# Performance work log

Measured on AMD Instinct MI355X. Metric: run time of the kernel, lower is better.

## Reference

```python
import jax, jax.numpy as jnp
import numpy as np

B = 128          # graphs
NPG = 512        # nodes per graph
N = B * NPG      # total nodes
DEG = 8
E = N * DEG      # total edges (intra-graph)
D = 100          # num_feature_dim / num_node_labels
HID = 128        # config.hidden
HEADS = 8
F1 = 20          # per-head dim of first GATConv in each GATNet
RATIO = 0.5
K = int(np.ceil(RATIO * NPG))  # nodes kept per graph by SAGPooling
NEG_SLOPE = 0.2


def setup_inputs() -> dict:
    key = jax.random.key(0)
    ks = jax.random.split(key, 24)
    x = jax.random.randint(ks[0], (N,), 0, D)
    # intra-graph random edges: local ids in [0, NPG) + graph offset
    src_l = jax.random.randint(ks[1], (B, NPG * DEG), 0, NPG)
    dst_l = jax.random.randint(ks[2], (B, NPG * DEG), 0, NPG)
    off = (jnp.arange(B) * NPG)[:, None]
    edge_index = jnp.stack([(src_l + off).ravel(), (dst_l + off).ravel()])
    batch = jnp.repeat(jnp.arange(B), NPG)

    def lin(k, fan_in, fan_out):
        return jax.random.normal(k, (fan_in, fan_out), jnp.float32) / np.sqrt(fan_in)

    def att(k, h, f):
        return jax.random.normal(k, (h, f), jnp.float32) * 0.1

    p = {
        # GATNet A (conv1): GATConv(D, 20, heads=8) then GATConv(160, HID, heads=1)
        "W_a1": lin(ks[3], D, HEADS * F1), "asrc_a1": att(ks[4], HEADS, F1),
        "adst_a1": att(ks[5], HEADS, F1), "b_a1": jnp.zeros((HEADS * F1,), jnp.float32),
        "W_a2": lin(ks[6], HEADS * F1, HID), "asrc_a2": att(ks[7], 1, HID),
        "adst_a2": att(ks[8], 1, HID), "b_a2": jnp.zeros((HID,), jnp.float32),
        # GATNet B (conv4): GATConv(HID, 20, heads=8) then GATConv(160, HID, heads=1)
        "W_b1": lin(ks[9], HID, HEADS * F1), "asrc_b1": att(ks[10], HEADS, F1),
        "adst_b1": att(ks[11], HEADS, F1), "b_b1": jnp.zeros((HEADS * F1,), jnp.float32),
        "W_b2": lin(ks[12], HEADS * F1, HID), "asrc_b2": att(ks[13], 1, HID),
        "adst_b2": att(ks[14], 1, HID), "b_b2": jnp.zeros((HID,), jnp.float32),
        # SAGPooling GraphConv(HID, 1)
        "w_rel": lin(ks[15], HID, 1), "w_root": lin(ks[16], HID, 1),
        "b_pool": jnp.zeros((1,), jnp.float32),
    }
    return {"x": x, "edge_index": edge_index, "batch": batch, **p}


def _gat_conv(h, src, dst, W, asrc, adst, b):
    """PyG GATConv (with self-loops already included in src/dst)."""
    Hh, Ff = asrc.shape
    z = (h @ W).reshape(N, Hh, Ff)                       # [N,H,F]
    es = jnp.sum(z * asrc, axis=-1)                      # [N,H] source logits
    ed = jnp.sum(z * adst, axis=-1)                      # [N,H] dest logits
    e = jax.nn.leaky_relu(es[src] + ed[dst], NEG_SLOPE)  # [E',H]
    m = jax.ops.segment_max(e, dst, num_segments=N)
    m = jnp.where(jnp.isfinite(m), m, 0.0)
    ex = jnp.exp(e - m[dst])
    den = jax.ops.segment_sum(ex, dst, num_segments=N)
    alpha = ex / (den[dst] + 1e-16)
    out = jax.ops.segment_sum(z[src] * alpha[:, :, None], dst, num_segments=N)
    return out.reshape(N, Hh * Ff) + b


def reference(x, edge_index, batch,
              W_a1, asrc_a1, adst_a1, b_a1, W_a2, asrc_a2, adst_a2, b_a2,
              W_b1, asrc_b1, adst_b1, b_b1, W_b2, asrc_b2, adst_b2, b_b2,
              w_rel, w_root, b_pool):
    src, dst = edge_index[0], edge_index[1]
    loops = jnp.arange(N)
    src_sl = jnp.concatenate([src, loops])  # GATConv adds self loops
    dst_sl = jnp.concatenate([dst, loops])

    h = jax.nn.one_hot(x, D, dtype=jnp.float32)
    # GATNet A: conv1 -> relu -> conv2 ; outer relu (dropout is eval no-op)
    h = jax.nn.relu(_gat_conv(h, src_sl, dst_sl, W_a1, asrc_a1, adst_a1, b_a1))
    h = _gat_conv(h, src_sl, dst_sl, W_a2, asrc_a2, adst_a2, b_a2)
    h = jax.nn.relu(h)
    # GATNet B
    h = jax.nn.relu(_gat_conv(h, src_sl, dst_sl, W_b1, asrc_b1, adst_b1, b_b1))
    h = _gat_conv(h, src_sl, dst_sl, W_b2, asrc_b2, adst_b2, b_b2)
    h = jax.nn.relu(h)

    # SAGPooling: GraphConv(HID,1) score (no self loops), tanh, per-graph top-k
    nbr = jax.ops.segment_sum(h[src], dst, num_segments=N)
    score = jnp.tanh(nbr @ w_rel + h @ w_root + b_pool).ravel()   # [N]
    sv, si = jax.lax.top_k(score.reshape(B, NPG), K)              # [B,K]
    perm = (si + (jnp.arange(B) * NPG)[:, None]).ravel()          # global node ids
    x_sel = h[perm] * sv.ravel()[:, None]                         # [B*K, HID]
    pooled = jnp.max(x_sel.reshape(B, K, HID), axis=1)            # global_max_pool
    batch_out = jnp.repeat(jnp.arange(B), K)
    return (pooled, perm, sv.ravel(), batch_out)
```

## Files before the change

kernel.cpp:

```cpp
#include <hip/hip_runtime.h>
#include <math.h>

#define N_NODES 65536
#define NPG     512
#define NGRAPH  128
#define E_EDGES 524288
#define MAXDEG  64
#define NHEADS  8
#define F1      20
#define HID     128
#define D160    160
#define KSEL    256
#define NLBL    100

typedef unsigned short ushort_t;
typedef unsigned int   uint_t;
typedef unsigned long long u64;
typedef __attribute__((ext_vector_type(8))) short short8;
typedef __attribute__((ext_vector_type(4))) float f32x4;

__device__ __forceinline__ float lrelu(float x){ return x > 0.f ? x : 0.2f*x; }
__device__ __forceinline__ ushort_t f2bf(float f){
    uint_t u = __float_as_uint(f);
    return (ushort_t)((u + 0x7FFFu + ((u >> 16) & 1u)) >> 16);
}
__device__ __forceinline__ float bf2f(ushort_t u){ return __uint_as_float(((uint_t)u) << 16); }
__device__ __forceinline__ float bflo(uint_t v){ return __uint_as_float(v << 16); }
__device__ __forceinline__ float bfhi(uint_t v){ return __uint_as_float(v & 0xFFFF0000u); }
__device__ __forceinline__ int xswz(int bid, int nblocks){
    return (bid & 7) * (nblocks >> 3) + (bid >> 3);
}
__device__ __forceinline__ float rdlanef(float v, int i){
    return __uint_as_float((uint_t)__builtin_amdgcn_readlane(__float_as_int(v), i));
}

__device__ __forceinline__ u64 comp_make(float s, int idx){
    uint_t u = __float_as_uint(s);
    u ^= (u & 0x80000000u) ? 0xFFFFFFFFu : 0x80000000u;
    return ((u64)u << 32) | (u64)(511 - idx);
}
__device__ __forceinline__ float comp_score(u64 c){
    uint_t u = (uint_t)(c >> 32);
    u ^= (u & 0x80000000u) ? 0x80000000u : 0xFFFFFFFFu;
    return __uint_as_float(u);
}
__device__ __forceinline__ int comp_idx(u64 c){ return 511 - (int)(c & 0x1FFu); }
__device__ __forceinline__ u64 shfl_xor_u64(u64 x, int m){
    uint_t lo = __shfl_xor((uint_t)x, m);
    uint_t hi = __shfl_xor((uint_t)(x >> 32), m);
    return ((u64)hi << 32) | lo;
}

__global__ void k_zero(uint4* __restrict__ p){
    p[blockIdx.x*blockDim.x + threadIdx.x] = (uint4){0,0,0,0};
}

__global__ void k_build_ell(const int* __restrict__ src, const int* __restrict__ dst,
                            int* __restrict__ deg, int* __restrict__ ell){
    int blk = xswz(blockIdx.x, E_EDGES/256);
    int e = blk*blockDim.x + threadIdx.x;
    int d = dst[e];
    int p = atomicAdd(&deg[d], 1);
    if(p < MAXDEG) ell[d*MAXDEG + p] = src[e];
}

__global__ void k_prep_a(const float* __restrict__ W, const float* __restrict__ asrc,
                         const float* __restrict__ adst,
                         ushort_t* __restrict__ Wbf, float* __restrict__ esT,
                         float* __restrict__ edT){
    int lbl = blockIdx.x;
    int f = threadIdx.x;
    const float* wrow = W + lbl*D160;
    Wbf[lbl*D160 + f] = f2bf(wrow[f]);
    if(f < 16){
        int h = f & 7;
        const float* av = ((f < 8) ? asrc : adst) + h*F1;
        float s = 0.f;
        #pragma unroll
        for(int k=0; k<F1; ++k) s += wrow[h*F1 + k]*av[k];
        if(f < 8) esT[lbl*8 + h] = s;
        else      edT[lbl*8 + h] = s;
    }
}

__global__ __launch_bounds__(256) void k_attn8_a(const int* __restrict__ x,
        const int* __restrict__ deg, const int* __restrict__ ell,
        const ushort_t* __restrict__ Wbf, const float* __restrict__ esT,
        const float* __restrict__ edT, const float* __restrict__ bias,
        ushort_t* __restrict__ out){
    __shared__ __align__(16) ushort_t Wl[NLBL*D160];
    __shared__ float esL[NLBL*8], edL[NLBL*8];
    int tid = threadIdx.x;
    for(int i = tid; i < NLBL*D160/8; i += 256)
        ((uint4*)Wl)[i] = ((const uint4*)Wbf)[i];
    for(int i = tid; i < NLBL*8; i += 256){ esL[i] = esT[i]; edL[i] = edT[i]; }
    __syncthreads();
    int blk = xswz(blockIdx.x, N_NODES*NHEADS/256);
    int t = blk*256 + tid;
    int n = t >> 3, h = t & 7;
    int dg = deg[n]; if(dg > MAXDEG) dg = MAXDEG;
    int lbl = x[n];
    float edn = edL[lbl*8 + h];
    float wself = expf(lrelu(esL[lbl*8 + h] + edn));
    float den = wself;
    float acc[F1];
    {
        const uint_t* zn = (const uint_t*)Wl + lbl*80 + h*10;
        #pragma unroll
        for(int f=0; f<10; ++f){
            uint_t v = zn[f];
            acc[2*f]   = wself*bflo(v);
            acc[2*f+1] = wself*bfhi(v);
        }
    }
    const int* el = ell + n*MAXDEG;
    int i = 0;
    for(; i+2 <= dg; i += 2){
        int sa = el[i], sb = el[i+1];
        int la = x[sa], lb = x[sb];
        float wa = expf(lrelu(esL[la*8 + h] + edn));
        float wb = expf(lrelu(esL[lb*8 + h] + edn));
        den += wa + wb;
        const uint_t* za = (const uint_t*)Wl + la*80 + h*10;
        const uint_t* zb = (const uint_t*)Wl + lb*80 + h*10;
        #pragma unroll
        for(int f=0; f<10; ++f){
            uint_t va = za[f], vb = zb[f];
            acc[2*f]   += wa*bflo(va) + wb*bflo(vb);
            acc[2*f+1] += wa*bfhi(va) + wb*bfhi(vb);
        }
    }
    if(i < dg){
        int sa = el[i];
        int la = x[sa];
        float wa = expf(lrelu(esL[la*8 + h] + edn));
        den += wa;
        const uint_t* za = (const uint_t*)Wl + la*80 + h*10;
        #pragma unroll
        for(int f=0; f<10; ++f){
            uint_t va = za[f];
            acc[2*f]   += wa*bflo(va);
            acc[2*f+1] += wa*bfhi(va);
        }
    }
    float inv = 1.f/(den + 1e-16f);
    uint_t* o = (uint_t*)(out + (size_t)n*D160 + h*F1);
    const float* bb = bias + h*F1;
    #pragma unroll
    for(int f=0; f<10; ++f){
        float v0 = fmaxf(acc[2*f]*inv   + bb[2*f],   0.f);
        float v1 = fmaxf(acc[2*f+1]*inv + bb[2*f+1], 0.f);
        o[f] = (uint_t)f2bf(v0) | ((uint_t)f2bf(v1) << 16);
    }
}

__global__ void k_attn8(const int* __restrict__ deg, const int* __restrict__ ell,
                        const ushort_t* __restrict__ z8, const float* __restrict__ es8,
                        const float* __restrict__ ed8, const float* __restrict__ bias,
                        ushort_t* __restrict__ out){
    int blk = xswz(blockIdx.x, N_NODES*NHEADS/256);
    int t = blk*blockDim.x + threadIdx.x;
    int n = t >> 3, h = t & 7;
    int dg = deg[n]; if(dg > MAXDEG) dg = MAXDEG;
    float edn = ed8[t];
    float wself = expf(lrelu(es8[t] + edn));
    float den = wself;
    float acc[F1];
    const uint_t* zn = (const uint_t*)(z8 + (size_t)n*D160 + h*F1);
    #pragma unroll
    for(int f=0; f<10; ++f){
        uint_t v = zn[f];
        acc[2*f]   = wself*bflo(v);
        acc[2*f+1] = wself*bfhi(v);
    }
    const int* el = ell + n*MAXDEG;
    int i = 0;
    for(; i+2 <= dg; i += 2){
        int sa = el[i], sb = el[i+1];
        float ea = es8[sa*NHEADS + h], eb = es8[sb*NHEADS + h];
        const uint_t* za = (const uint_t*)(z8 + (size_t)sa*D160 + h*F1);
        const uint_t* zb = (const uint_t*)(z8 + (size_t)sb*D160 + h*F1);
        float wa = expf(lrelu(ea + edn));
        float wb = expf(lrelu(eb + edn));
        den += wa + wb;
        #pragma unroll
        for(int f=0; f<10; ++f){
            uint_t va = za[f], vb = zb[f];
            acc[2*f]   += wa*bflo(va) + wb*bflo(vb);
            acc[2*f+1] += wa*bfhi(va) + wb*bfhi(vb);
        }
    }
    if(i < dg){
        int sa = el[i];
        float ea = es8[sa*NHEADS + h];
        const uint_t* za = (const uint_t*)(z8 + (size_t)sa*D160 + h*F1);
        float wa = expf(lrelu(ea + edn));
        den += wa;
        #pragma unroll
        for(int f=0; f<10; ++f){
            uint_t va = za[f];
            acc[2*f]   += wa*bflo(va);
            acc[2*f+1] += wa*bfhi(va);
        }
    }
    float inv = 1.f/(den + 1e-16f);
    uint_t* o = (uint_t*)(out + (size_t)n*D160 + h*F1);
    const float* bb = bias + h*F1;
    #pragma unroll
    for(int f=0; f<10; ++f){
        float v0 = fmaxf(acc[2*f]*inv   + bb[2*f],   0.f);
        float v1 = fmaxf(acc[2*f+1]*inv + bb[2*f+1], 0.f);
        o[f] = (uint_t)f2bf(v0) | ((uint_t)f2bf(v1) << 16);
    }
}

template<int IN, int OUT, bool DOT>
__global__ __launch_bounds__(256) void k_gemm_mfma(const ushort_t* __restrict__ A,
                                                   const float* __restrict__ W,
                                                   ushort_t* __restrict__ C,
                                                   const float* __restrict__ va,
                                                   const float* __restrict__ vb,
                                                   float* __restrict__ oa,
                                                   float* __restrict__ ob){
    constexpr int NT = OUT/16;
    constexpr int KS = IN/32;
    constexpr int LDW = IN + 8;
    __shared__ __align__(16) ushort_t Wt[OUT*LDW];
    int tid = threadIdx.x;
    for(int i = tid; i < IN*OUT; i += 256){
        int k = i / OUT, n = i - k*OUT;
        Wt[n*LDW + k] = f2bf(W[i]);
    }
    __syncthreads();
    int blk = xswz(blockIdx.x, N_NODES/64);
    int wave = tid >> 6, lane = tid & 63;
    int col16 = lane & 15;
    int kq = (lane >> 4) * 8;
    int row = blk*64 + wave*16 + col16;
    const ushort_t* Ar = A + (size_t)row*IN + kq;
    f32x4 acc[NT];
    #pragma unroll
    for(int c=0;c<NT;++c) acc[c] = (f32x4){0.f,0.f,0.f,0.f};
    #pragma unroll
    for(int ks=0; ks<KS; ++ks){
        short8 af = *reinterpret_cast<const short8*>(Ar + ks*32);
        #pragma unroll
        for(int c=0;c<NT;++c){
            short8 bf = *reinterpret_cast<const short8*>(&Wt[(c*16 + col16)*LDW + ks*32 + kq]);
            acc[c] = __builtin_amdgcn_mfma_f32_16x16x32_bf16(af, bf, acc[c], 0, 0, 0);
        }
    }
    int rbase = blk*64 + wave*16 + (lane >> 4)*4;
    #pragma unroll
    for(int c=0;c<NT;++c){
        #pragma unroll
        for(int r=0;r<4;++r){
            C[(size_t)(rbase + r)*OUT + c*16 + col16] = f2bf(acc[c][r]);
        }
    }
    if(DOT){
        float pa[4] = {0,0,0,0}, pb[4] = {0,0,0,0};
        #pragma unroll
        for(int c=0;c<NT;++c){
            float a = va[c*16 + col16];
            float b = vb[c*16 + col16];
            #pragma unroll
            for(int r=0;r<4;++r){ pa[r] += acc[c][r]*a; pb[r] += acc[c][r]*b; }
        }
        #pragma unroll
        for(int o=1;o<16;o<<=1){
            #pragma unroll
            for(int r=0;r<4;++r){ pa[r] += __shfl_xor(pa[r], o); pb[r] += __shfl_xor(pb[r], o); }
        }
        if(col16 == 0){
            #pragma unroll
            for(int r=0;r<4;++r){ oa[rbase + r] = pa[r]; ob[rbase + r] = pb[r]; }
        }
    }
}

__global__ __launch_bounds__(256) void k_gemm_b1(const ushort_t* __restrict__ A,
                                                 const float* __restrict__ W,
                                                 const float* __restrict__ asrc,
                                                 const float* __restrict__ adst,
                                                 ushort_t* __restrict__ C,
                                                 float* __restrict__ es8,
                                                 float* __restrict__ ed8){
    constexpr int IN = HID, OUTW = D160, NT = 11, KS = IN/32, LDW = IN + 8;
    __shared__ __align__(16) ushort_t Wt[(OUTW+16)*LDW];
    int tid = threadIdx.x;
    for(int i = tid; i < IN*OUTW; i += 256){
        int k = i / OUTW, n = i - k*OUTW;
        Wt[n*LDW + k] = f2bf(W[i]);
    }
    for(int i = tid; i < IN*16; i += 256){
        int k = i >> 4, j = i & 15;
        const float* av = (j < 8 ? asrc : adst) + (j & 7)*F1;
        const float* wr = W + k*OUTW + (j & 7)*F1;
        float s = 0.f;
        #pragma unroll
        for(int f=0; f<F1; ++f) s += wr[f]*av[f];
        Wt[(OUTW + j)*LDW + k] = f2bf(s);
    }
    __syncthreads();
    int blk = xswz(blockIdx.x, N_NODES/64);
    int wave = tid >> 6, lane = tid & 63;
    int col16 = lane & 15;
    int kq = (lane >> 4) * 8;
    int row = blk*64 + wave*16 + col16;
    const ushort_t* Ar = A + (size_t)row*IN + kq;
    f32x4 acc[NT];
    #pragma unroll
    for(int c=0;c<NT;++c) acc[c] = (f32x4){0.f,0.f,0.f,0.f};
    #pragma unroll
    for(int ks=0; ks<KS; ++ks){
        short8 af = *reinterpret_cast<const short8*>(Ar + ks*32);
        #pragma unroll
        for(int c=0;c<NT;++c){
            short8 bf = *reinterpret_cast<const short8*>(&Wt[(c*16 + col16)*LDW + ks*32 + kq]);
            acc[c] = __builtin_amdgcn_mfma_f32_16x16x32_bf16(af, bf, acc[c], 0, 0, 0);
        }
    }
    int rbase = blk*64 + wave*16 + (lane >> 4)*4;
    #pragma unroll
    for(int c=0;c<10;++c){
        #pragma unroll
        for(int r=0;r<4;++r){
            C[(size_t)(rbase + r)*OUTW + c*16 + col16] = f2bf(acc[c][r]);
        }
    }
    #pragma unroll
    for(int r=0;r<4;++r){
        float v = acc[10][r];
        if(col16 < 8) es8[(size_t)(rbase + r)*8 + col16] = v;
        else          ed8[(size_t)(rbase + r)*8 + (col16 - 8)] = v;
    }
}

template<typename OutT, bool DOT>
__global__ void k_attn1(const int* __restrict__ deg, const int* __restrict__ ell,
                        const ushort_t* __restrict__ Z, const float* __restrict__ es,
                        const float* __restrict__ ed, const float* __restrict__ bias,
                        OutT* __restrict__ out,
                        const float* __restrict__ wa, const float* __restrict__ wb,
                        float* __restrict__ oa, float* __restrict__ ob){
    int blk = xswz(blockIdx.x, N_NODES/4);
    int gt = blk*blockDim.x + threadIdx.x;
    int n = gt >> 6;
    int l = threadIdx.x & 63;
    int dg = deg[n]; if(dg > MAXDEG) dg = MAXDEG;
    float edn = ed[n];
    float wself = expf(lrelu(es[n] + edn));
    int s_l = 0; float w_l = 0.f;
    if(l < dg){ s_l = ell[n*MAXDEG + l]; w_l = expf(lrelu(es[s_l] + edn)); }
    float den = w_l;
    for(int o=32;o>0;o>>=1) den += __shfl_xor(den,o);
    den += wself;
    const uint_t* Zu = (const uint_t*)Z;
    uint_t zn = Zu[(size_t)n*64 + l];
    float acc0 = wself*bflo(zn);
    float acc1 = wself*bfhi(zn);
    int i = 0;
    for(; i+4 <= dg; i += 4){
        int s0 = __builtin_amdgcn_readlane(s_l, i);
        int s1 = __builtin_amdgcn_readlane(s_l, i+1);
        int s2 = __builtin_amdgcn_readlane(s_l, i+2);
        int s3 = __builtin_amdgcn_readlane(s_l, i+3);
        uint_t z0 = Zu[(size_t)s0*64 + l];
        uint_t z1 = Zu[(size_t)s1*64 + l];
        uint_t z2 = Zu[(size_t)s2*64 + l];
        uint_t z3 = Zu[(size_t)s3*64 + l];
        float w0 = rdlanef(w_l, i);
        float w1 = rdlanef(w_l, i+1);
        float w2 = rdlanef(w_l, i+2);
        float w3 = rdlanef(w_l, i+3);
        acc0 += w0*bflo(z0) + w1*bflo(z1);
        acc1 += w0*bfhi(z0) + w1*bfhi(z1);
        acc0 += w2*bflo(z2) + w3*bflo(z3);
        acc1 += w2*bfhi(z2) + w3*bfhi(z3);
    }
    for(; i < dg; ++i){
        int s0 = __builtin_amdgcn_readlane(s_l, i);
        float w0 = rdlanef(w_l, i);
        uint_t z0 = Zu[(size_t)s0*64 + l];
        acc0 += w0*bflo(z0);
        acc1 += w0*bfhi(z0);
    }
    float inv = 1.f/(den + 1e-16f);
    float2 bb = ((const float2*)bias)[l];
    float r0 = fmaxf(acc0*inv + bb.x, 0.f);
    float r1 = fmaxf(acc1*inv + bb.y, 0.f);
    if(sizeof(OutT) == 2){
        ((uint_t*)out)[(size_t)n*64 + l] = (uint_t)f2bf(r0) | ((uint_t)f2bf(r1) << 16);
    } else {
        float2 rv; rv.x = r0; rv.y = r1;
        ((float2*)out)[(size_t)n*64 + l] = rv;
    }
    if(DOT){
        float2 a2 = ((const float2*)wa)[l];
        float2 b2 = ((const float2*)wb)[l];
        float pa = r0*a2.x + r1*a2.y;
        float pb = r0*b2.x + r1*b2.y;
        for(int o=32;o>0;o>>=1){ pa += __shfl_xor(pa,o); pb += __shfl_xor(pb,o); }
        if(l==0){ oa[n] = pa; ob[n] = pb; }
    }
}

__global__ void k_score(const int* __restrict__ deg, const int* __restrict__ ell,
                        const float* __restrict__ yrel, const float* __restrict__ rroot,
                        const float* __restrict__ bpool, float* __restrict__ score){
    int blk = xswz(blockIdx.x, N_NODES/256);
    int n = blk*blockDim.x + threadIdx.x;
    int dg = deg[n]; if(dg > MAXDEG) dg = MAXDEG;
    float s = rroot[n] + bpool[0];
    const int* el = ell + n*MAXDEG;
    int i = 0;
    for(; i+4 <= dg; i += 4){
        float y0 = yrel[el[i]],   y1 = yrel[el[i+1]];
        float y2 = yrel[el[i+2]], y3 = yrel[el[i+3]];
        s += (y0 + y1) + (y2 + y3);
    }
    for(; i < dg; ++i) s += yrel[el[i]];
    score[n] = tanhf(s);
}

__global__ __launch_bounds__(512) void k_topk_pool(const float* __restrict__ score,
                                                   const ushort_t* __restrict__ H,
                                                   float* __restrict__ pooled,
                                                   float* __restrict__ perm_f,
                                                   float* __restrict__ sv,
                                                   float* __restrict__ batch_f){
    __shared__ int   sidx[KSEL];
    __shared__ float sval[KSEL];
    __shared__ float pmax[512];
    int g = xswz(blockIdx.x, NGRAPH);
    int base = g*NPG;
    int t = threadIdx.x;
    if(t < 64){
        int l = t;
        u64 v[8];
        #pragma unroll
        for(int r=0;r<8;++r){
            int i = r*64 + l;
            v[r] = comp_make(score[base + i], i);
        }
        #pragma unroll
        for(int kk=1; kk<=9; ++kk){
            int k = 1 << kk;
            #pragma unroll
            for(int jj=kk-1; jj>=0; --jj){
                int j = 1 << jj;
                if(j < 64){
                    bool lower = (l & j) == 0;
                    #pragma unroll
                    for(int r=0;r<8;++r){
                        int i = r*64 + l;
                        u64 p = shfl_xor_u64(v[r], j);
                        bool desc = (i & k) == 0;
                        u64 mx = v[r] > p ? v[r] : p;
                        u64 mn = v[r] > p ? p : v[r];
                        v[r] = (lower == desc) ? mx : mn;
                    }
                } else {
                    int jr = j >> 6;
                    #pragma unroll
                    for(int r=0;r<8;++r){
                        if((r & jr) == 0){
                            int rp = r | jr;
                            int i = r*64 + l;
                            bool desc = (i & k) == 0;
                            u64 a = v[r], b = v[rp];
                            u64 mx = a > b ? a : b;
                            u64 mn = a > b ? b : a;
                            v[r]  = desc ? mx : mn;
                            v[rp] = desc ? mn : mx;
                        }
                    }
                }
            }
        }
        #pragma unroll
        for(int r=0;r<4;++r){
            int i = r*64 + l;
            int idx = comp_idx(v[r]);
            float s = comp_score(v[r]);
            perm_f[g*KSEL + i]  = (float)(base + idx);
            sv[g*KSEL + i]      = s;
            batch_f[g*KSEL + i] = (float)g;
            sidx[i] = idx; sval[i] = s;
        }
    }
    __syncthreads();
    int c = t & 127, kc = t >> 7;
    float mx = -1e30f;
    for(int kk = kc*64; kk < kc*64 + 64; ++kk){
        mx = fmaxf(mx, bf2f(H[(size_t)(base + sidx[kk])*HID + c]) * sval[kk]);
    }
    pmax[t] = mx;
    __syncthreads();
    if(t < HID){
        pooled[g*HID + t] = fmaxf(fmaxf(pmax[t], pmax[t+128]),
                                  fmaxf(pmax[t+256], pmax[t+384]));
    }
}

extern "C" void kernel_launch(void* const* d_in, const int* in_sizes, int n_in,
                              void* d_out, int out_size, void* d_ws, size_t ws_size,
                              hipStream_t stream) {
    const int*   x       = (const int*)  d_in[0];
    const int*   eidx    = (const int*)  d_in[1];
    const float* W_a1    = (const float*)d_in[3];
    const float* asrc_a1 = (const float*)d_in[4];
    const float* adst_a1 = (const float*)d_in[5];
    const float* b_a1    = (const float*)d_in[6];
    const float* W_a2    = (const float*)d_in[7];
    const float* asrc_a2 = (const float*)d_in[8];
    const float* adst_a2 = (const float*)d_in[9];
    const float* b_a2    = (const float*)d_in[10];
    const float* W_b1    = (const float*)d_in[11];
    const float* asrc_b1 = (const float*)d_in[12];
    const float* adst_b1 = (const float*)d_in[13];
    const float* b_b1    = (const float*)d_in[14];
    const float* W_b2    = (const float*)d_in[15];
    const float* asrc_b2 = (const float*)d_in[16];
    const float* adst_b2 = (const float*)d_in[17];
    const float* b_b2    = (const float*)d_in[18];
    const float* w_rel   = (const float*)d_in[19];
    const float* w_root  = (const float*)d_in[20];
    const float* b_pool  = (const float*)d_in[21];

    const int* e_src = eidx;
    const int* e_dst = eidx + E_EDGES;

    char* ws = (char*)d_ws;
    size_t off = 0;
    auto alloc = [&](size_t bytes)->char*{
        char* p = ws + off;
        off += (bytes + 255) & ~(size_t)255;
        return p;
    };
    int*      deg   = (int*)     alloc((size_t)N_NODES*4);
    int*      ell   = (int*)     alloc((size_t)N_NODES*MAXDEG*4);
    ushort_t* z8    = (ushort_t*)alloc((size_t)N_NODES*D160*2);
    ushort_t* h8    = (ushort_t*)alloc((size_t)N_NODES*D160*2);
    ushort_t* zc    = (ushort_t*)alloc((size_t)N_NODES*HID*2);
    ushort_t* hmid  = (ushort_t*)alloc((size_t)N_NODES*HID*2);
    ushort_t* hfin  = (ushort_t*)alloc((size_t)N_NODES*HID*2);
    float*    es8   = (float*)   alloc((size_t)N_NODES*NHEADS*4);
    float*    ed8   = (float*)   alloc((size_t)N_NODES*NHEADS*4);
    float*    es1   = (float*)   alloc((size_t)N_NODES*4);
    float*    ed1   = (float*)   alloc((size_t)N_NODES*4);
    float*    yrel  = (float*)   alloc((size_t)N_NODES*4);
    float*    rroot = (float*)   alloc((size_t)N_NODES*4);
    float*    score = (float*)   alloc((size_t)N_NODES*4);
    ushort_t* Wbf   = (ushort_t*)alloc((size_t)NLBL*D160*2);
    float*    esT   = (float*)   alloc((size_t)NLBL*8*4);
    float*    edT   = (float*)   alloc((size_t)NLBL*8*4);
    (void)ws_size; (void)n_in; (void)in_sizes; (void)out_size;

    float* out      = (float*)d_out;
    float* pooled   = out;
    float* perm_f   = out + NGRAPH*HID;
    float* sv       = perm_f + NGRAPH*KSEL;
    float* batch_f  = sv + NGRAPH*KSEL;

    k_zero<<<N_NODES*4/(16*256), 256, 0, stream>>>((uint4*)deg);
    k_build_ell<<<E_EDGES/256, 256, 0, stream>>>(e_src, e_dst, deg, ell);

    k_prep_a<<<NLBL, D160, 0, stream>>>(W_a1, asrc_a1, adst_a1, Wbf, esT, edT);
    k_attn8_a<<<N_NODES*NHEADS/256, 256, 0, stream>>>(x, deg, ell, Wbf, esT, edT, b_a1, h8);

    k_gemm_mfma<D160, HID, true><<<N_NODES/64, 256, 0, stream>>>(h8, W_a2, zc, asrc_a2, adst_a2, es1, ed1);
    k_attn1<ushort_t, false><<<N_NODES/4, 256, 0, stream>>>(deg, ell, zc, es1, ed1, b_a2, hmid,
                                                            nullptr, nullptr, nullptr, nullptr);

    k_gemm_b1<<<N_NODES/64, 256, 0, stream>>>(hmid, W_b1, asrc_b1, adst_b1, z8, es8, ed8);
    k_attn8<<<N_NODES*NHEADS/256, 256, 0, stream>>>(deg, ell, z8, es8, ed8, b_b1, h8);

    k_gemm_mfma<D160, HID, true><<<N_NODES/64, 256, 0, stream>>>(h8, W_b2, zc, asrc_b2, adst_b2, es1, ed1);
    k_attn1<ushort_t, true><<<N_NODES/4, 256, 0, stream>>>(deg, ell, zc, es1, ed1, b_b2, hfin,
                                                           w_rel, w_root, yrel, rroot);

    k_score<<<N_NODES/256, 256, 0, stream>>>(deg, ell, yrel, rroot, b_pool, score);
    k_topk_pool<<<NGRAPH, NPG, 0, stream>>>(score, hfin, pooled, perm_f, sv, batch_f);
}
```

Before: 240.5 us.

## Precompute padded bf16 weight images once and fold attention vectors into GEMM columns

A single prep kernel now zeroes the degree array and builds transposed, padded bf16 weight images for all three dense layers. The attention projections (W·a_src, W·a_dst) are folded in as extra output columns, so the GEMMs produce es/ed directly from the MFMA accumulators instead of a shuffle-reduced dot product. Each of the 1024 GEMM blocks now copies the ready image into LDS with vector loads rather than redoing fp32→bf16 conversion and transpose, and the A fragments are loaded before the weight copy to overlap latency. In exchange, es/ed are computed with bf16-rounded folded weights, and the 128-wide GEMMs gain an extra 16-column MFMA tile.

```diff
diff --git a/kernel.cpp b/kernel.cpp
--- a/kernel.cpp
+++ b/kernel.cpp
@@ -13,6 +13,16 @@
 #define KSEL    256
 #define NLBL    100
 
+#define IMG_A2_ELEMS (144*168)
+#define IMG_B1_ELEMS (176*136)
+#define PB_ZERO 0
+#define PB_A2   64
+#define PB_B1   (PB_A2 + 95)
+#define PB_B2   (PB_B1 + 94)
+#define PB_WA1  (PB_B2 + 95)
+#define PB_EST  (PB_WA1 + 63)
+#define PB_TOT  (PB_EST + 7)
+
 typedef unsigned short ushort_t;
 typedef unsigned int   uint_t;
 typedef unsigned long long u64;
@@ -51,8 +61,77 @@
     return ((u64)hi << 32) | lo;
 }
 
-__global__ void k_zero(uint4* __restrict__ p){
-    p[blockIdx.x*blockDim.x + threadIdx.x] = (uint4){0,0,0,0};
+__global__ void k_prep(const float* __restrict__ Wa1, const float* __restrict__ as1,
+                       const float* __restrict__ ad1,
+                       const float* __restrict__ Wa2, const float* __restrict__ as2,
+                       const float* __restrict__ ad2,
+                       const float* __restrict__ Wb1, const float* __restrict__ asb1,
+                       const float* __restrict__ adb1,
+                       const float* __restrict__ Wb2, const float* __restrict__ asb2,
+                       const float* __restrict__ adb2,
+                       int* __restrict__ deg,
+                       ushort_t* __restrict__ imgA2, ushort_t* __restrict__ imgB1,
+                       ushort_t* __restrict__ imgB2,
+                       ushort_t* __restrict__ Wbf, float* __restrict__ esT,
+                       float* __restrict__ edT){
+    int bid = blockIdx.x, tid = threadIdx.x;
+    if(bid < PB_A2){
+        ((uint4*)deg)[(bid - PB_ZERO)*256 + tid] = (uint4){0,0,0,0};
+    } else if(bid < PB_B1 || (bid >= PB_B2 && bid < PB_WA1)){
+        bool isB2 = (bid >= PB_B2);
+        int j = (bid - (isB2 ? PB_B2 : PB_A2))*256 + tid;
+        if(j < IMG_A2_ELEMS){
+            const float* W  = isB2 ? Wb2 : Wa2;
+            const float* as = isB2 ? asb2 : as2;
+            const float* ad = isB2 ? adb2 : ad2;
+            int n = j / 168, k = j - n*168;
+            float v = 0.f;
+            if(k < 160){
+                if(n < 128) v = W[k*128 + n];
+                else if(n < 130){
+                    const float* av = (n == 128) ? as : ad;
+                    float s = 0.f;
+                    for(int c=0; c<128; ++c) s += W[k*128 + c]*av[c];
+                    v = s;
+                }
+            }
+            (isB2 ? imgB2 : imgA2)[j] = f2bf(v);
+        }
+    } else if(bid < PB_B2){
+        int j = (bid - PB_B1)*256 + tid;
+        if(j < IMG_B1_ELEMS){
+            int n = j / 136, k = j - n*136;
+            float v = 0.f;
+            if(k < 128){
+                if(n < 160) v = Wb1[k*160 + n];
+                else {
+                    int j2 = n - 160, h = j2 & 7;
+                    const float* av = ((j2 < 8) ? asb1 : adb1) + h*F1;
+                    const float* wr = Wb1 + k*160 + h*F1;
+                    float s = 0.f;
+                    #pragma unroll
+                    for(int f=0; f<F1; ++f) s += wr[f]*av[f];
+                    v = s;
+                }
+            }
+            imgB1[j] = f2bf(v);
+        }
+    } else if(bid < PB_EST){
+        int j = (bid - PB_WA1)*256 + tid;
+        if(j < NLBL*D160) Wbf[j] = f2bf(Wa1[j]);
+    } else {
+        int t = (bid - PB_EST)*256 + tid;
+        if(t < NLBL*16){
+            int lbl = t >> 4, j = t & 15, h = j & 7;
+            const float* av = ((j < 8) ? as1 : ad1) + h*F1;
+            const float* wr = Wa1 + lbl*D160 + h*F1;
+            float s = 0.f;
+            #pragma unroll
+            for(int f=0; f<F1; ++f) s += wr[f]*av[f];
+            if(j < 8) esT[lbl*8 + h] = s;
+            else      edT[lbl*8 + h] = s;
+        }
+    }
 }
 
 __global__ void k_build_ell(const int* __restrict__ src, const int* __restrict__ dst,
@@ -62,25 +141,6 @@
     int d = dst[e];
     int p = atomicAdd(&deg[d], 1);
     if(p < MAXDEG) ell[d*MAXDEG + p] = src[e];
-}
-
-__global__ void k_prep_a(const float* __restrict__ W, const float* __restrict__ asrc,
-                         const float* __restrict__ adst,
-                         ushort_t* __restrict__ Wbf, float* __restrict__ esT,
-                         float* __restrict__ edT){
-    int lbl = blockIdx.x;
-    int f = threadIdx.x;
-    const float* wrow = W + lbl*D160;
-    Wbf[lbl*D160 + f] = f2bf(wrow[f]);
-    if(f < 16){
-        int h = f & 7;
-        const float* av = ((f < 8) ? asrc : adst) + h*F1;
-        float s = 0.f;
-        #pragma unroll
-        for(int k=0; k<F1; ++k) s += wrow[h*F1 + k]*av[k];
-        if(f < 8) esT[lbl*8 + h] = s;
-        else      edT[lbl*8 + h] = s;
-    }
 }
 
 __global__ __launch_bounds__(256) void k_attn8_a(const int* __restrict__ x,
@@ -214,126 +274,67 @@
     }
 }
 
-template<int IN, int OUT, bool DOT>
-__global__ __launch_bounds__(256) void k_gemm_mfma(const ushort_t* __restrict__ A,
-                                                   const float* __restrict__ W,
-                                                   ushort_t* __restrict__ C,
-                                                   const float* __restrict__ va,
-                                                   const float* __restrict__ vb,
-                                                   float* __restrict__ oa,
-                                                   float* __restrict__ ob){
-    constexpr int NT = OUT/16;
+template<int IN, int OUTC, int OUTIMG, bool ESED8>
+__global__ __launch_bounds__(256) void k_gemm2(const ushort_t* __restrict__ Wimg,
+                                               const ushort_t* __restrict__ A,
+                                               ushort_t* __restrict__ C,
+                                               float* __restrict__ oa,
+                                               float* __restrict__ ob){
+    constexpr int LDW = IN + 8;
+    constexpr int NT = OUTIMG/16;
+    constexpr int NC = OUTC/16;
     constexpr int KS = IN/32;
-    constexpr int LDW = IN + 8;
-    __shared__ __align__(16) ushort_t Wt[OUT*LDW];
+    constexpr int ELEMS = OUTIMG*LDW;
+    __shared__ __align__(16) ushort_t Wt[ELEMS];
     int tid = threadIdx.x;
-    for(int i = tid; i < IN*OUT; i += 256){
-        int k = i / OUT, n = i - k*OUT;
-        Wt[n*LDW + k] = f2bf(W[i]);
-    }
-    __syncthreads();
     int blk = xswz(blockIdx.x, N_NODES/64);
     int wave = tid >> 6, lane = tid & 63;
     int col16 = lane & 15;
     int kq = (lane >> 4) * 8;
     int row = blk*64 + wave*16 + col16;
     const ushort_t* Ar = A + (size_t)row*IN + kq;
+    short8 afr[KS];
+    #pragma unroll
+    for(int ks=0; ks<KS; ++ks)
+        afr[ks] = *reinterpret_cast<const short8*>(Ar + ks*32);
+    for(int i = tid; i < ELEMS/8; i += 256)
+        ((uint4*)Wt)[i] = ((const uint4*)Wimg)[i];
+    __syncthreads();
     f32x4 acc[NT];
     #pragma unroll
     for(int c=0;c<NT;++c) acc[c] = (f32x4){0.f,0.f,0.f,0.f};
     #pragma unroll
     for(int ks=0; ks<KS; ++ks){
-        short8 af = *reinterpret_cast<const short8*>(Ar + ks*32);
         #pragma unroll
         for(int c=0;c<NT;++c){
             short8 bf = *reinterpret_cast<const short8*>(&Wt[(c*16 + col16)*LDW + ks*32 + kq]);
-            acc[c] = __builtin_amdgcn_mfma_f32_16x16x32_bf16(af, bf, acc[c], 0, 0, 0);
+            acc[c] = __builtin_amdgcn_mfma_f32_16x16x32_bf16(afr[ks], bf, acc[c], 0, 0, 0);
         }
     }
     int rbase = blk*64 + wave*16 + (lane >> 4)*4;
     #pragma unroll
-    for(int c=0;c<NT;++c){
+    for(int c=0;c<NC;++c){
         #pragma unroll
         for(int r=0;r<4;++r){
-            C[(size_t)(rbase + r)*OUT + c*16 + col16] = f2bf(acc[c][r]);
-        }
-    }
-    if(DOT){
-        float pa[4] = {0,0,0,0}, pb[4] = {0,0,0,0};
-        #pragma unroll
-        for(int c=0;c<NT;++c){
-            float a = va[c*16 + col16];
-            float b = vb[c*16 + col16];
-            #pragma unroll
-            for(int r=0;r<4;++r){ pa[r] += acc[c][r]*a; pb[r] += acc[c][r]*b; }
-        }
-        #pragma unroll
-        for(int o=1;o<16;o<<=1){
-            #pragma unroll
-            for(int r=0;r<4;++r){ pa[r] += __shfl_xor(pa[r], o); pb[r] += __shfl_xor(pb[r], o); }
-        }
+            C[(size_t)(rbase + r)*OUTC + c*16 + col16] = f2bf(acc[c][r]);
+        }
+    }
+    if(ESED8){
+        #pragma unroll
+        for(int r=0;r<4;++r){
+            float v = acc[NT-1][r];
+            if(col16 < 8) oa[(size_t)(rbase + r)*8 + col16] = v;
+            else          ob[(size_t)(rbase + r)*8 + (col16 - 8)] = v;
+        }
+    } else {
         if(col16 == 0){
             #pragma unroll
-            for(int r=0;r<4;++r){ oa[rbase + r] = pa[r]; ob[rbase + r] = pb[r]; }
-        }
-    }
-}
-
-__global__ __launch_bounds__(256) void k_gemm_b1(const ushort_t* __restrict__ A,
-                                                 const float* __restrict__ W,
-                                                 const float* __restrict__ asrc,
-                                                 const float* __restrict__ adst,
-                                                 ushort_t* __restrict__ C,
-                                                 float* __restrict__ es8,
-                                                 float* __restrict__ ed8){
-    constexpr int IN = HID, OUTW = D160, NT = 11, KS = IN/32, LDW = IN + 8;
-    __shared__ __align__(16) ushort_t Wt[(OUTW+16)*LDW];
-    int tid = threadIdx.x;
-    for(int i = tid; i < IN*OUTW; i += 256){
-        int k = i / OUTW, n = i - k*OUTW;
-        Wt[n*LDW + k] = f2bf(W[i]);
-    }
-    for(int i = tid; i < IN*16; i += 256){
-        int k = i >> 4, j = i & 15;
-        const float* av = (j < 8 ? asrc : adst) + (j & 7)*F1;
-        const float* wr = W + k*OUTW + (j & 7)*F1;
-        float s = 0.f;
-        #pragma unroll
-        for(int f=0; f<F1; ++f) s += wr[f]*av[f];
-        Wt[(OUTW + j)*LDW + k] = f2bf(s);
-    }
-    __syncthreads();
-    int blk = xswz(blockIdx.x, N_NODES/64);
-    int wave = tid >> 6, lane = tid & 63;
-    int col16 = lane & 15;
-    int kq = (lane >> 4) * 8;
-    int row = blk*64 + wave*16 + col16;
-    const ushort_t* Ar = A + (size_t)row*IN + kq;
-    f32x4 acc[NT];
-    #pragma unroll
-    for(int c=0;c<NT;++c) acc[c] = (f32x4){0.f,0.f,0.f,0.f};
-    #pragma unroll
-    for(int ks=0; ks<KS; ++ks){
-        short8 af = *reinterpret_cast<const short8*>(Ar + ks*32);
-        #pragma unroll
-        for(int c=0;c<NT;++c){
-            short8 bf = *reinterpret_cast<const short8*>(&Wt[(c*16 + col16)*LDW + ks*32 + kq]);
-            acc[c] = __builtin_amdgcn_mfma_f32_16x16x32_bf16(af, bf, acc[c], 0, 0, 0);
-        }
-    }
-    int rbase = blk*64 + wave*16 + (lane >> 4)*4;
-    #pragma unroll
-    for(int c=0;c<10;++c){
-        #pragma unroll
-        for(int r=0;r<4;++r){
-            C[(size_t)(rbase + r)*OUTW + c*16 + col16] = f2bf(acc[c][r]);
-        }
-    }
-    #pragma unroll
-    for(int r=0;r<4;++r){
-        float v = acc[10][r];
-        if(col16 < 8) es8[(size_t)(rbase + r)*8 + col16] = v;
-        else          ed8[(size_t)(rbase + r)*8 + (col16 - 8)] = v;
+            for(int r=0;r<4;++r) oa[rbase + r] = acc[NT-1][r];
+        }
+        if(col16 == 1){
+            #pragma unroll
+            for(int r=0;r<4;++r) ob[rbase + r] = acc[NT-1][r];
+        }
     }
 }
 
@@ -539,23 +540,26 @@
         off += (bytes + 255) & ~(size_t)255;
         return p;
     };
-    int*      deg   = (int*)     alloc((size_t)N_NODES*4);
-    int*      ell   = (int*)     alloc((size_t)N_NODES*MAXDEG*4);
-    ushort_t* z8    = (ushort_t*)alloc((size_t)N_NODES*D160*2);
-    ushort_t* h8    = (ushort_t*)alloc((size_t)N_NODES*D160*2);
-    ushort_t* zc    = (ushort_t*)alloc((size_t)N_NODES*HID*2);
-    ushort_t* hmid  = (ushort_t*)alloc((size_t)N_NODES*HID*2);
-    ushort_t* hfin  = (ushort_t*)alloc((size_t)N_NODES*HID*2);
-    float*    es8   = (float*)   alloc((size_t)N_NODES*NHEADS*4);
-    float*    ed8   = (float*)   alloc((size_t)N_NODES*NHEADS*4);
-    float*    es1   = (float*)   alloc((size_t)N_NODES*4);
-    float*    ed1   = (float*)   alloc((size_t)N_NODES*4);
-    float*    yrel  = (float*)   alloc((size_t)N_NODES*4);
-    float*    rroot = (float*)   alloc((size_t)N_NODES*4);
-    float*    score = (float*)   alloc((size_t)N_NODES*4);
-    ushort_t* Wbf   = (ushort_t*)alloc((size_t)NLBL*D160*2);
-    float*    esT   = (float*)   alloc((size_t)NLBL*8*4);
-    float*    edT   = (float*)   alloc((size_t)NLBL*8*4);
+    int*      deg    = (int*)     alloc((size_t)N_NODES*4);
+    int*      ell    = (int*)     alloc((size_t)N_NODES*MAXDEG*4);
+    ushort_t* z8     = (ushort_t*)alloc((size_t)N_NODES*D160*2);
+    ushort_t* h8     = (ushort_t*)alloc((size_t)N_NODES*D160*2);
+    ushort_t* zc     = (ushort_t*)alloc((size_t)N_NODES*HID*2);
+    ushort_t* hmid   = (ushort_t*)alloc((size_t)N_NODES*HID*2);
+    ushort_t* hfin   = (ushort_t*)alloc((size_t)N_NODES*HID*2);
+    float*    es8    = (float*)   alloc((size_t)N_NODES*NHEADS*4);
+    float*    ed8    = (float*)   alloc((size_t)N_NODES*NHEADS*4);
+    float*    es1    = (float*)   alloc((size_t)N_NODES*4);
+    float*    ed1    = (float*)   alloc((size_t)N_NODES*4);
+    float*    yrel   = (float*)   alloc((size_t)N_NODES*4);
+    float*    rroot  = (float*)   alloc((size_t)N_NODES*4);
+    float*    score  = (float*)   alloc((size_t)N_NODES*4);
+    ushort_t* Wbf    = (ushort_t*)alloc((size_t)NLBL*D160*2);
+    float*    esT    = (float*)   alloc((size_t)NLBL*8*4);
+    float*    edT    = (float*)   alloc((size_t)NLBL*8*4);
+    ushort_t* imgA2  = (ushort_t*)alloc((size_t)IMG_A2_ELEMS*2);
+    ushort_t* imgB1  = (ushort_t*)alloc((size_t)IMG_B1_ELEMS*2);
+    ushort_t* imgB2  = (ushort_t*)alloc((size_t)IMG_A2_ELEMS*2);
     (void)ws_size; (void)n_in; (void)in_sizes; (void)out_size;
 
     float* out      = (float*)d_out;
@@ -564,20 +568,23 @@
     float* sv       = perm_f + NGRAPH*KSEL;
     float* batch_f  = sv + NGRAPH*KSEL;
 
-    k_zero<<<N_NODES*4/(16*256), 256, 0, stream>>>((uint4*)deg);
+    k_prep<<<PB_TOT, 256, 0, stream>>>(W_a1, asrc_a1, adst_a1,
+                                       W_a2, asrc_a2, adst_a2,
+                                       W_b1, asrc_b1, adst_b1,
+                                       W_b2, asrc_b2, adst_b2,
+                                       deg, imgA2, imgB1, imgB2, Wbf, esT, edT);
     k_build_ell<<<E_EDGES/256, 256, 0, stream>>>(e_src, e_dst, deg, ell);
 
-    k_prep_a<<<NLBL, D160, 0, stream>>>(W_a1, asrc_a1, adst_a1, Wbf, esT, edT);
     k_attn8_a<<<N_NODES*NHEADS/256, 256, 0, stream>>>(x, deg, ell, Wbf, esT, edT, b_a1, h8);
 
-    k_gemm_mfma<D160, HID, true><<<N_NODES/64, 256, 0, stream>>>(h8, W_a2, zc, asrc_a2, adst_a2, es1, ed1);
+    k_gemm2<D160, HID, 144, false><<<N_NODES/64, 256, 0, stream>>>(imgA2, h8, zc, es1, ed1);
     k_attn1<ushort_t, false><<<N_NODES/4, 256, 0, stream>>>(deg, ell, zc, es1, ed1, b_a2, hmid,
                                                             nullptr, nullptr, nullptr, nullptr);
 
-    k_gemm_b1<<<N_NODES/64, 256, 0, stream>>>(hmid, W_b1, asrc_b1, adst_b1, z8, es8, ed8);
+    k_gemm2<HID, D160, 176, true><<<N_NODES/64, 256, 0, stream>>>(imgB1, hmid, z8, es8, ed8);
     k_attn8<<<N_NODES*NHEADS/256, 256, 0, stream>>>(deg, ell, z8, es8, ed8, b_b1, h8);
 
-    k_gemm_mfma<D160, HID, true><<<N_NODES/64, 256, 0, stream>>>(h8, W_b2, zc, asrc_b2, adst_b2, es1, ed1);
+    k_gemm2<D160, HID, 144, false><<<N_NODES/64, 256, 0, stream>>>(imgB2, h8, zc, es1, ed1);
     k_attn1<ushort_t, true><<<N_NODES/4, 256, 0, stream>>>(deg, ell, zc, es1, ed1, b_b2, hfin,
                                                            w_rel, w_root, yrel, rroot);
 
```

After: 226.4 us. -5.9%, faster.
